# Kernel optimization log

Measured on AMD Instinct MI355X. Metric: run time of the kernel, lower is better.

The kernel has to match this reference:

```python
import jax, jax.numpy as jnp
import numpy as np

N_E = 8192
E_DIM = 256
BETA = 0.1


def setup_inputs() -> dict:
    key = jax.random.key(0)
    k1, k2 = jax.random.split(key)
    z = jax.random.normal(k1, (16, E_DIM, 2048), dtype=jnp.float32)  # B,C,L
    # embedding init: uniform(-1/n_e, 1/n_e)
    codebook = jax.random.uniform(k2, (N_E, E_DIM), dtype=jnp.float32,
                                  minval=-1.0 / N_E, maxval=1.0 / N_E)
    return {"z": z, "codebook": codebook}


def reference(z, codebook):
    B, C, L = z.shape
    zt = jnp.transpose(z, (0, 2, 1))          # B,L,C
    zf = zt.reshape(-1, C)                    # BL,C
    # squared-distance via expansion: |z|^2 + |e|^2 - 2 z.e
    d = (jnp.sum(zf * zf, axis=1, keepdims=True)
         + jnp.sum(codebook * codebook, axis=1)
         - 2.0 * jnp.einsum('bd,nd->bn', zf, codebook))  # BL,N
    inds = jnp.argmin(d, axis=1)              # BL
    z_q = codebook[inds].reshape(B, L, C)     # B,L,C
    sg = jax.lax.stop_gradient
    loss = (BETA * jnp.mean((sg(z_q) - zt) ** 2)
            + jnp.mean((z_q - sg(zt)) ** 2))
    # straight-through estimator
    z_q = zt + sg(z_q - zt)
    z_q = jnp.transpose(z_q, (0, 2, 1))       # B,C,L
    return z_q, loss, inds
```

## Files before the change

### kernel.cpp

```cpp
#include <hip/hip_runtime.h>
#include <math.h>

#define NE    8192
#define EDIM  256
#define LDIM  2048
#define BL    32768
#define ZQ_SIZE 8388608
#define LOSS_IDX ZQ_SIZE
#define INDS_OFF (ZQ_SIZE + 1)

#define BT_HI_F 0
#define BT_LO_F 1048576
#define PART_F  2097152
#define SZ_F    6291456
#define AT_LO_SH 8388608

typedef __attribute__((ext_vector_type(8))) short short8;
typedef __attribute__((ext_vector_type(16))) float float16v;

__device__ __forceinline__ unsigned short f2bf(float f) {
    unsigned u = __float_as_uint(f);
    return (unsigned short)((u + 0x7FFFu + ((u >> 16) & 1u)) >> 16);
}
__device__ __forceinline__ float bf2f(unsigned short h) {
    return __uint_as_float(((unsigned)h) << 16);
}
__device__ __forceinline__ void pmerge(ulonglong2& a, const ulonglong2 b) {
    unsigned long long lo = a.x < b.x ? a.x : b.x;
    unsigned long long hi = a.x < b.x ? b.x : a.x;
    unsigned long long s2 = a.y < b.y ? a.y : b.y;
    a.x = lo; a.y = s2 < hi ? s2 : hi;
}
__device__ __forceinline__ void gload_lds16(const void* g, void* l) {
    __builtin_amdgcn_global_load_lds(
        (const __attribute__((address_space(1))) unsigned int*)g,
        (__attribute__((address_space(3))) unsigned int*)l, 16, 0, 0);
}

__global__ void vq_bsplit_kernel(const float* __restrict__ cb, float* __restrict__ out) {
    unsigned short* Bth = (unsigned short*)(out + BT_HI_F);
    unsigned short* Btl = (unsigned short*)(out + BT_LO_F);
    const int oct = blockIdx.y;
    const int row = blockIdx.x * 256 + threadIdx.x;
    const float* src = cb + (size_t)row * EDIM + oct * 8;
    float v[8];
    *(float4*)&v[0] = *(const float4*)src;
    *(float4*)&v[4] = *(const float4*)(src + 4);
    short8 h8, l8;
    #pragma unroll
    for (int j = 0; j < 8; ++j) {
        unsigned short h = f2bf(v[j]);
        h8[j] = (short)h;
        l8[j] = (short)f2bf(v[j] - bf2f(h));
    }
    size_t o = ((size_t)(oct * NE + row)) << 3;
    *(short8*)(Bth + o) = h8;
    *(short8*)(Btl + o) = l8;
}

__global__ void vq_szsplit_kernel(const float* __restrict__ z, float* __restrict__ out,
                                  unsigned short* __restrict__ ws) {
    __shared__ double Sd[4][128];
    unsigned short* Ath = ws;
    unsigned short* Atl = ws + AT_LO_SH;
    const int t  = threadIdx.x;
    const int ql = t & 127;
    const int cq = t >> 7;
    const int q  = blockIdx.x * 128 + ql;
    if (q == 0 && cq == 0) out[LOSS_IDX] = 0.0f;
    const int b = q >> 11, l = q & 2047;
    const float* zb = z + (size_t)b * EDIM * LDIM + l;
    double acc = 0.0;
    #pragma unroll 2
    for (int og = cq * 8; og < cq * 8 + 8; ++og) {
        float v[8];
        #pragma unroll
        for (int j = 0; j < 8; ++j) v[j] = zb[(size_t)(og * 8 + j) * LDIM];
        short8 h8, l8;
        #pragma unroll
        for (int j = 0; j < 8; ++j) {
            unsigned u  = __float_as_uint(v[j]);
            unsigned hu = u & 0xFFFF0000u;
            float rem   = v[j] - __uint_as_float(hu);
            h8[j] = (short)(hu >> 16);
            l8[j] = (short)(__float_as_uint(rem) >> 16);
            double dv = (double)v[j];
            acc = fma(dv, dv, acc);
        }
        size_t o = ((size_t)og * BL + q) << 3;
        *(short8*)(Ath + o) = h8;
        *(short8*)(Atl + o) = l8;
    }
    Sd[cq][ql] = acc;
    __syncthreads();
    if (t < 128) {
        double s = Sd[0][t] + Sd[1][t] + Sd[2][t] + Sd[3][t];
        out[SZ_F + blockIdx.x * 128 + t] = (float)s;
    }
}

__global__ void vq_sz_kernel(const float* __restrict__ z, float* __restrict__ out) {
    const int q = blockIdx.x * 256 + threadIdx.x;
    if (q == 0) out[LOSS_IDX] = 0.0f;
    const int b = q >> 11, l = q & 2047;
    const float* zb = z + (size_t)b * EDIM * LDIM + l;
    double acc = 0.0;
    #pragma unroll 8
    for (int c = 0; c < EDIM; ++c) {
        double v = (double)zb[(size_t)c * LDIM];
        acc = fma(v, v, acc);
    }
    out[SZ_F + q] = (float)acc;
}

__global__ __launch_bounds__(512, 4) void vq_mfma_ws_kernel(
        const unsigned short* __restrict__ ws, float* __restrict__ out) {
    __shared__ __align__(16) unsigned short AhS[4 * 128 * 8];
    __shared__ __align__(16) unsigned short AlS[4 * 128 * 8];
    __shared__ __align__(16) unsigned short BhS[4 * 256 * 8];
    __shared__ __align__(16) unsigned short BlS[4 * 256 * 8];

    const unsigned short* Ath = ws;
    const unsigned short* Atl = ws + AT_LO_SH;
    const unsigned short* Bth = (const unsigned short*)(out + BT_HI_F);
    const unsigned short* Btl = (const unsigned short*)(out + BT_LO_F);
    const float* Szp = out + SZ_F;
    ulonglong2* part = (ulonglong2*)(out + PART_F);

    const int t    = threadIdx.x;
    const int lane = t & 63;
    const int wave = t >> 6;
    const int l31  = lane & 31;
    const int khal = lane >> 5;
    const int wm   = wave >> 2;
    const int wn   = wave & 3;

    const int q0 = (blockIdx.x >> 1) * 128;
    const int nh = blockIdx.x & 1;

    float szv2[2];
    #pragma unroll
    for (int ct = 0; ct < 2; ++ct)
        szv2[ct] = Szp[q0 + wm * 64 + ct * 32 + l31];

    float16v acc[2][2];
    unsigned long long k1r[2], k2r[2];
    #pragma unroll
    for (int ct = 0; ct < 2; ++ct) { k1r[ct] = ~0ull; k2r[ct] = ~0ull; }

    for (int cl = 0; cl < 16; ++cl) {
        const int n0c = nh * 4096 + cl * 256;
        #pragma unroll
        for (int rt = 0; rt < 2; ++rt)
            #pragma unroll
            for (int ct = 0; ct < 2; ++ct)
                #pragma unroll
                for (int e = 0; e < 16; ++e)
                    acc[rt][ct][e] = 0.f;

        for (int ks = 0; ks < 8; ++ks) {
            __syncthreads();
            #pragma unroll
            for (int i = 0; i < 2; ++i) {
                const int s   = wave * 2 + i;
                const int arr = s >> 3;
                const int oc  = (s >> 1) & 3;
                const int mh  = s & 1;
                const unsigned short* src = (arr ? Atl : Ath)
                    + ((size_t)((ks * 4 + oc) * BL + q0 + mh * 64 + lane) << 3);
                unsigned short* dst = (arr ? AlS : AhS)
                    + (((oc << 7) + mh * 64 + lane) << 3);
                gload_lds16(src, dst);
            }
            #pragma unroll
            for (int p = 0; p < 4; ++p) {
                const int s   = wave * 4 + p;
                const int arr = s >> 4;
                const int oc  = (s >> 2) & 3;
                const int seg = s & 3;
                const int og  = ks * 4 + oc;
                const unsigned short* src = (arr ? Btl : Bth)
                    + ((size_t)(og * NE + n0c + seg * 64 + lane) << 3);
                unsigned short* dst = (arr ? BlS : BhS)
                    + (((oc << 8) + seg * 64 + lane) << 3);
                gload_lds16(src, dst);
            }
            __syncthreads();
            #pragma unroll
            for (int c = 0; c < 2; ++c) {
                const int oct = c * 2 + khal;
                short8 cbh[2], cbl[2], qh[2], ql[2];
                #pragma unroll
                for (int rt = 0; rt < 2; ++rt) {
                    const int n = wn * 64 + rt * 32 + l31;
                    cbh[rt] = *(const short8*)&BhS[((oct << 8) + n) << 3];
                    cbl[rt] = *(const short8*)&BlS[((oct << 8) + n) << 3];
                }
                #pragma unroll
                for (int ct = 0; ct < 2; ++ct) {
                    const int m = wm * 64 + ct * 32 + l31;
                    qh[ct] = *(const short8*)&AhS[((oct << 7) + m) << 3];
                    ql[ct] = *(const short8*)&AlS[((oct << 7) + m) << 3];
                }
                #pragma unroll
                for (int rt = 0; rt < 2; ++rt)
                    #pragma unroll
                    for (int ct = 0; ct < 2; ++ct) {
                        acc[rt][ct] = __builtin_amdgcn_mfma_f32_32x32x16_bf16(cbh[rt], qh[ct], acc[rt][ct], 0, 0, 0);
                        acc[rt][ct] = __builtin_amdgcn_mfma_f32_32x32x16_bf16(cbl[rt], qh[ct], acc[rt][ct], 0, 0, 0);
                        acc[rt][ct] = __builtin_amdgcn_mfma_f32_32x32x16_bf16(cbh[rt], ql[ct], acc[rt][ct], 0, 0, 0);
                    }
            }
        }
        #pragma unroll
        for (int ct = 0; ct < 2; ++ct) {
            #pragma unroll
            for (int rt = 0; rt < 2; ++rt) {
                #pragma unroll
                for (int e = 0; e < 16; ++e) {
                    float s = fmaf(-2.0f, acc[rt][ct][e], szv2[ct]);
                    unsigned u = __float_as_uint(s);
                    unsigned mono = u ^ ((unsigned)(((int)u) >> 31) | 0x80000000u);
                    const int n = n0c + wn * 64 + rt * 32
                                + (e & 3) + 8 * (e >> 2) + 4 * khal;
                    unsigned long long k = ((unsigned long long)mono << 32) | (unsigned)n;
                    if (k < k1r[ct]) { k2r[ct] = k1r[ct]; k1r[ct] = k; }
                    else if (k < k2r[ct]) { k2r[ct] = k; }
                }
            }
        }
    }

    __syncthreads();
    ulonglong2* Sm = (ulonglong2*)AhS;
    #pragma unroll
    for (int ct = 0; ct < 2; ++ct) {
        unsigned long long k1 = k1r[ct], k2 = k2r[ct];
        unsigned long long o1 = __shfl_xor(k1, 32, 64);
        unsigned long long o2 = __shfl_xor(k2, 32, 64);
        unsigned long long lo = k1 < o1 ? k1 : o1;
        unsigned long long hi = k1 < o1 ? o1 : k1;
        k2 = k2 < o2 ? k2 : o2;
        k2 = k2 < hi ? k2 : hi;
        k1 = lo;
        if (khal == 0) {
            const int ql_ = wm * 64 + ct * 32 + l31;
            ulonglong2 v; v.x = k1; v.y = k2;
            Sm[(ql_ << 2) + wn] = v;
        }
    }
    __syncthreads();
    if (t < 128) {
        ulonglong2 p = Sm[(t << 2) + 0];
        pmerge(p, Sm[(t << 2) + 1]);
        pmerge(p, Sm[(t << 2) + 2]);
        pmerge(p, Sm[(t << 2) + 3]);
        part[(size_t)nh * BL + q0 + t] = p;
    }
}

__global__ __launch_bounds__(512, 4) void vq_mfma_kernel(
        const float* __restrict__ z, float* __restrict__ out) {
    __shared__ __align__(16) unsigned short AhS[4 * 128 * 8];
    __shared__ __align__(16) unsigned short AlS[4 * 128 * 8];
    __shared__ __align__(16) unsigned short BhS[4 * 256 * 8];
    __shared__ __align__(16) unsigned short BlS[4 * 256 * 8];

    const unsigned short* Bth = (const unsigned short*)(out + BT_HI_F);
    const unsigned short* Btl = (const unsigned short*)(out + BT_LO_F);
    const float* Szp = out + SZ_F;
    ulonglong2* part = (ulonglong2*)(out + PART_F);

    const int t    = threadIdx.x;
    const int lane = t & 63;
    const int wave = t >> 6;
    const int l31  = lane & 31;
    const int khal = lane >> 5;
    const int wm   = wave >> 2;
    const int wn   = wave & 3;

    const int q0 = (blockIdx.x >> 1) * 128;
    const int nh = blockIdx.x & 1;
    const int b  = q0 >> 11;
    const int l0 = q0 & 2047;
    const float* zbase = z + (size_t)b * (EDIM * LDIM) + l0;

    float szv2[2];
    #pragma unroll
    for (int ct = 0; ct < 2; ++ct)
        szv2[ct] = Szp[q0 + wm * 64 + ct * 32 + l31];

    const int am  = t & 127;
    const int aog = t >> 7;

    float16v acc[2][2];
    unsigned long long k1r[2], k2r[2];
    #pragma unroll
    for (int ct = 0; ct < 2; ++ct) { k1r[ct] = ~0ull; k2r[ct] = ~0ull; }

    for (int cl = 0; cl < 16; ++cl) {
        const int n0c = nh * 4096 + cl * 256;
        #pragma unroll
        for (int rt = 0; rt < 2; ++rt)
            #pragma unroll
            for (int ct = 0; ct < 2; ++ct)
                #pragma unroll
                for (int e = 0; e < 16; ++e)
                    acc[rt][ct][e] = 0.f;

        for (int ks = 0; ks < 8; ++ks) {
            const int kc = ks * 32;
            __syncthreads();
            {
                const float* asrc = zbase + (size_t)(kc + aog * 8) * LDIM + am;
                float av[8];
                #pragma unroll
                for (int j = 0; j < 8; ++j) av[j] = asrc[(size_t)j * LDIM];
                short8 h8, l8;
                #pragma unroll
                for (int j = 0; j < 8; ++j) {
                    unsigned u  = __float_as_uint(av[j]);
                    unsigned hu = u & 0xFFFF0000u;
                    float rem   = av[j] - __uint_as_float(hu);
                    h8[j] = (short)(hu >> 16);
                    l8[j] = (short)(__float_as_uint(rem) >> 16);
                }
                *(short8*)&AhS[((aog << 7) + am) << 3] = h8;
                *(short8*)&AlS[((aog << 7) + am) << 3] = l8;
            }
            #pragma unroll
            for (int p = 0; p < 4; ++p) {
                const int s   = wave * 4 + p;
                const int arr = s >> 4;
                const int oc  = (s >> 2) & 3;
                const int seg = s & 3;
                const int og  = ks * 4 + oc;
                const unsigned short* src = (arr ? Btl : Bth)
                    + ((size_t)(og * NE + n0c + seg * 64 + lane) << 3);
                unsigned short* dst = (arr ? BlS : BhS)
                    + (((oc << 8) + seg * 64 + lane) << 3);
                gload_lds16(src, dst);
            }
            __syncthreads();
            #pragma unroll
            for (int c = 0; c < 2; ++c) {
                const int oct = c * 2 + khal;
                short8 cbh[2], cbl[2], qh[2], ql[2];
                #pragma unroll
                for (int rt = 0; rt < 2; ++rt) {
                    const int n = wn * 64 + rt * 32 + l31;
                    cbh[rt] = *(const short8*)&BhS[((oct << 8) + n) << 3];
                    cbl[rt] = *(const short8*)&BlS[((oct << 8) + n) << 3];
                }
                #pragma unroll
                for (int ct = 0; ct < 2; ++ct) {
                    const int m = wm * 64 + ct * 32 + l31;
                    qh[ct] = *(const short8*)&AhS[((oct << 7) + m) << 3];
                    ql[ct] = *(const short8*)&AlS[((oct << 7) + m) << 3];
                }
                #pragma unroll
                for (int rt = 0; rt < 2; ++rt)
                    #pragma unroll
                    for (int ct = 0; ct < 2; ++ct) {
                        acc[rt][ct] = __builtin_amdgcn_mfma_f32_32x32x16_bf16(cbh[rt], qh[ct], acc[rt][ct], 0, 0, 0);
                        acc[rt][ct] = __builtin_amdgcn_mfma_f32_32x32x16_bf16(cbl[rt], qh[ct], acc[rt][ct], 0, 0, 0);
                        acc[rt][ct] = __builtin_amdgcn_mfma_f32_32x32x16_bf16(cbh[rt], ql[ct], acc[rt][ct], 0, 0, 0);
                    }
            }
        }
        #pragma unroll
        for (int ct = 0; ct < 2; ++ct) {
            #pragma unroll
            for (int rt = 0; rt < 2; ++rt) {
                #pragma unroll
                for (int e = 0; e < 16; ++e) {
                    float s = fmaf(-2.0f, acc[rt][ct][e], szv2[ct]);
                    unsigned u = __float_as_uint(s);
                    unsigned mono = u ^ ((unsigned)(((int)u) >> 31) | 0x80000000u);
                    const int n = n0c + wn * 64 + rt * 32
                                + (e & 3) + 8 * (e >> 2) + 4 * khal;
                    unsigned long long k = ((unsigned long long)mono << 32) | (unsigned)n;
                    if (k < k1r[ct]) { k2r[ct] = k1r[ct]; k1r[ct] = k; }
                    else if (k < k2r[ct]) { k2r[ct] = k; }
                }
            }
        }
    }

    __syncthreads();
    ulonglong2* Sm = (ulonglong2*)AhS;
    #pragma unroll
    for (int ct = 0; ct < 2; ++ct) {
        unsigned long long k1 = k1r[ct], k2 = k2r[ct];
        unsigned long long o1 = __shfl_xor(k1, 32, 64);
        unsigned long long o2 = __shfl_xor(k2, 32, 64);
        unsigned long long lo = k1 < o1 ? k1 : o1;
        unsigned long long hi = k1 < o1 ? o1 : k1;
        k2 = k2 < o2 ? k2 : o2;
        k2 = k2 < hi ? k2 : hi;
        k1 = lo;
        if (khal == 0) {
            const int ql_ = wm * 64 + ct * 32 + l31;
            ulonglong2 v; v.x = k1; v.y = k2;
            Sm[(ql_ << 2) + wn] = v;
        }
    }
    __syncthreads();
    if (t < 128) {
        ulonglong2 p = Sm[(t << 2) + 0];
        pmerge(p, Sm[(t << 2) + 1]);
        pmerge(p, Sm[(t << 2) + 2]);
        pmerge(p, Sm[(t << 2) + 3]);
        part[(size_t)nh * BL + q0 + t] = p;
    }
}

__global__ void vq_verify_kernel(const float* __restrict__ z,
                                 const float* __restrict__ cb,
                                 float* __restrict__ out) {
    const int t    = threadIdx.x;
    const int w    = t >> 6;
    const int lane = t & 63;
    const int q    = blockIdx.x * 4 + w;
    const int b    = q >> 11, l = q & 2047;
    const ulonglong2* part = (const ulonglong2*)(out + PART_F);
    ulonglong2 g = part[q];
    pmerge(g, part[(size_t)BL + q]);
    const int c1 = (int)(unsigned)(g.x & 0xFFFFFFFFull);
    const int c2 = (int)(unsigned)(g.y & 0xFFFFFFFFull);
    const float szq = out[SZ_F + q];
    const float* zb = z + (size_t)b * EDIM * LDIM + l;
    const float* r1 = cb + (size_t)c1 * EDIM;
    const float* r2 = cb + (size_t)c2 * EDIM;
    double d1 = 0.0, d2 = 0.0;
    #pragma unroll
    for (int j = 0; j < 4; ++j) {
        int d = lane + 64 * j;
        double zv = (double)zb[(size_t)d * LDIM];
        d1 = fma(zv, (double)r1[d], d1);
        d2 = fma(zv, (double)r2[d], d2);
    }
    #pragma unroll
    for (int off = 32; off; off >>= 1) {
        d1 += __shfl_xor(d1, off, 64);
        d2 += __shfl_xor(d2, off, 64);
    }
    if (lane == 0) {
        float s1 = fmaf(-2.0f, (float)d1, szq);
        float s2 = fmaf(-2.0f, (float)d2, szq);
        int win = (s1 < s2) ? c1 : (s2 < s1 ? c2 : (c1 < c2 ? c1 : c2));
        out[INDS_OFF + q] = (float)win;
    }
}

__global__ void vq_output_kernel(const float* __restrict__ z,
                                 const float* __restrict__ cb,
                                 float* __restrict__ out) {
    __shared__ float rows[32 * 257];
    __shared__ float wsum[4];
    const float* indsf = out + INDS_OFF;
    const int t  = threadIdx.x;
    const int i0 = blockIdx.x * 32;
    const int b  = i0 >> 11;
    const int l0 = i0 & 2047;
    {
        int r  = t >> 3;
        int fb = t & 7;
        int idx = (int)indsf[i0 + r];
        const float* crow = cb + (size_t)idx * EDIM;
        #pragma unroll
        for (int j = 0; j < 8; ++j) {
            int f = fb + 8 * j;
            float4 v = *(const float4*)(crow + 4 * f);
            float* dst = &rows[r * 257 + 4 * f];
            dst[0] = v.x; dst[1] = v.y; dst[2] = v.z; dst[3] = v.w;
        }
    }
    __syncthreads();
    const int l  = t & 31;
    const int c0 = t >> 5;
    const size_t base = (size_t)b * EDIM * LDIM + l0 + l;
    float lsum = 0.0f;
    #pragma unroll 4
    for (int cc = 0; cc < 32; ++cc) {
        int c = c0 + 8 * cc;
        float q  = rows[l * 257 + c];
        float zv = z[base + (size_t)c * LDIM];
        float d  = q - zv;
        out[base + (size_t)c * LDIM] = zv + d;
        lsum += d * d;
    }
    #pragma unroll
    for (int off = 32; off; off >>= 1) lsum += __shfl_xor(lsum, off, 64);
    if ((t & 63) == 0) wsum[t >> 6] = lsum;
    __syncthreads();
    if (t == 0) {
        float s = wsum[0] + wsum[1] + wsum[2] + wsum[3];
        atomicAdd(out + LOSS_IDX, s * (1.1f / (float)ZQ_SIZE));
    }
}

extern "C" void kernel_launch(void* const* d_in, const int* in_sizes, int n_in,
                              void* d_out, int out_size, void* d_ws, size_t ws_size,
                              hipStream_t stream) {
    const float* z  = (const float*)d_in[0];
    const float* cb = (const float*)d_in[1];
    float* out = (float*)d_out;

    const bool use_ws = (d_ws != nullptr) && (ws_size >= (size_t)33554432);

    vq_bsplit_kernel<<<dim3(32, 32),   dim3(256), 0, stream>>>(cb, out);
    if (use_ws) {
        unsigned short* ws = (unsigned short*)d_ws;
        vq_szsplit_kernel<<<dim3(256),     dim3(512), 0, stream>>>(z, out, ws);
        vq_mfma_ws_kernel<<<dim3(BL / 64), dim3(512), 0, stream>>>(ws, out);
    } else {
        vq_sz_kernel    <<<dim3(BL / 256), dim3(256), 0, stream>>>(z, out);
        vq_mfma_kernel  <<<dim3(BL / 64),  dim3(512), 0, stream>>>(z, out);
    }
    vq_verify_kernel<<<dim3(BL / 4),   dim3(256), 0, stream>>>(z, cb, out);
    vq_output_kernel<<<dim3(BL / 32),  dim3(256), 0, stream>>>(z, cb, out);
}
```

Baseline: 572.2 us.

## Triple-buffer LDS tiles with a single barrier per k-step in VQ MFMA kernel

Replaces the double-synchronized load/compute loop with a three-stage LDS ring buffer. Each k-substep now covers two octets, and the next stage's global-to-LDS copy is issued before computing on the current one. The code waits with a partial vmcnt plus one barrier, raises wave priority around the MFMA block, and fully unrolls the codebook chunk loop through macros. The goal is to hide global load latency and halve barrier count. In exchange it uses more LDS, which may reduce occupancy, and adds subtle indexing and wait-count logic across stages.

```diff
diff --git a/kernel.cpp b/kernel.cpp
--- a/kernel.cpp
+++ b/kernel.cpp
@@ -115,10 +115,7 @@
 
 __global__ __launch_bounds__(512, 4) void vq_mfma_ws_kernel(
         const unsigned short* __restrict__ ws, float* __restrict__ out) {
-    __shared__ __align__(16) unsigned short AhS[4 * 128 * 8];
-    __shared__ __align__(16) unsigned short AlS[4 * 128 * 8];
-    __shared__ __align__(16) unsigned short BhS[4 * 256 * 8];
-    __shared__ __align__(16) unsigned short BlS[4 * 256 * 8];
+    __shared__ __align__(16) unsigned short L[3 * 12288];
 
     const unsigned short* Ath = ws;
     const unsigned short* Atl = ws + AT_LO_SH;
@@ -137,102 +134,128 @@
 
     const int q0 = (blockIdx.x >> 1) * 128;
     const int nh = blockIdx.x & 1;
+    const int nh4096 = nh * 4096;
 
     float szv2[2];
     #pragma unroll
     for (int ct = 0; ct < 2; ++ct)
         szv2[ct] = Szp[q0 + wm * 64 + ct * 32 + l31];
 
+    const int a_arr = t >> 8;
+    const int a_oc2 = (t >> 7) & 1;
+    const int a_m   = t & 127;
+    const unsigned short* a_srcb = (a_arr ? Atl : Ath)
+        + ((size_t)(a_oc2 * BL + q0 + a_m) << 3);
+    unsigned short* a_dstb = L + a_arr * 2048 + (((a_oc2 << 7) + a_m) << 3);
+    const unsigned short* b_srcb[2];
+    unsigned short* b_dstb[2];
+    #pragma unroll
+    for (int p = 0; p < 2; ++p) {
+        const int idx = t + p * 512;
+        const int arr = idx >> 9;
+        const int oc2 = (idx >> 8) & 1;
+        const int n   = idx & 255;
+        b_srcb[p] = (arr ? Btl : Bth) + ((size_t)(oc2 * NE + n) << 3);
+        b_dstb[p] = L + 4096 + arr * 4096 + (((oc2 << 8) + n) << 3);
+    }
+
     float16v acc[2][2];
     unsigned long long k1r[2], k2r[2];
     #pragma unroll
     for (int ct = 0; ct < 2; ++ct) { k1r[ct] = ~0ull; k2r[ct] = ~0ull; }
 
-    for (int cl = 0; cl < 16; ++cl) {
-        const int n0c = nh * 4096 + cl * 256;
-        #pragma unroll
-        for (int rt = 0; rt < 2; ++rt)
-            #pragma unroll
-            for (int ct = 0; ct < 2; ++ct)
-                #pragma unroll
-                for (int e = 0; e < 16; ++e)
-                    acc[rt][ct][e] = 0.f;
-
-        for (int ks = 0; ks < 8; ++ks) {
-            __syncthreads();
-            #pragma unroll
-            for (int i = 0; i < 2; ++i) {
-                const int s   = wave * 2 + i;
-                const int arr = s >> 3;
-                const int oc  = (s >> 1) & 3;
-                const int mh  = s & 1;
-                const unsigned short* src = (arr ? Atl : Ath)
-                    + ((size_t)((ks * 4 + oc) * BL + q0 + mh * 64 + lane) << 3);
-                unsigned short* dst = (arr ? AlS : AhS)
-                    + (((oc << 7) + mh * 64 + lane) << 3);
-                gload_lds16(src, dst);
-            }
-            #pragma unroll
-            for (int p = 0; p < 4; ++p) {
-                const int s   = wave * 4 + p;
-                const int arr = s >> 4;
-                const int oc  = (s >> 2) & 3;
-                const int seg = s & 3;
-                const int og  = ks * 4 + oc;
-                const unsigned short* src = (arr ? Btl : Bth)
-                    + ((size_t)(og * NE + n0c + seg * 64 + lane) << 3);
-                unsigned short* dst = (arr ? BlS : BhS)
-                    + (((oc << 8) + seg * 64 + lane) << 3);
-                gload_lds16(src, dst);
-            }
-            __syncthreads();
-            #pragma unroll
-            for (int c = 0; c < 2; ++c) {
-                const int oct = c * 2 + khal;
-                short8 cbh[2], cbl[2], qh[2], ql[2];
-                #pragma unroll
-                for (int rt = 0; rt < 2; ++rt) {
-                    const int n = wn * 64 + rt * 32 + l31;
-                    cbh[rt] = *(const short8*)&BhS[((oct << 8) + n) << 3];
-                    cbl[rt] = *(const short8*)&BlS[((oct << 8) + n) << 3];
-                }
-                #pragma unroll
-                for (int ct = 0; ct < 2; ++ct) {
-                    const int m = wm * 64 + ct * 32 + l31;
-                    qh[ct] = *(const short8*)&AhS[((oct << 7) + m) << 3];
-                    ql[ct] = *(const short8*)&AlS[((oct << 7) + m) << 3];
-                }
-                #pragma unroll
-                for (int rt = 0; rt < 2; ++rt)
-                    #pragma unroll
-                    for (int ct = 0; ct < 2; ++ct) {
-                        acc[rt][ct] = __builtin_amdgcn_mfma_f32_32x32x16_bf16(cbh[rt], qh[ct], acc[rt][ct], 0, 0, 0);
-                        acc[rt][ct] = __builtin_amdgcn_mfma_f32_32x32x16_bf16(cbl[rt], qh[ct], acc[rt][ct], 0, 0, 0);
-                        acc[rt][ct] = __builtin_amdgcn_mfma_f32_32x32x16_bf16(cbh[rt], ql[ct], acc[rt][ct], 0, 0, 0);
-                    }
-            }
-        }
-        #pragma unroll
-        for (int ct = 0; ct < 2; ++ct) {
-            #pragma unroll
-            for (int rt = 0; rt < 2; ++rt) {
-                #pragma unroll
-                for (int e = 0; e < 16; ++e) {
-                    float s = fmaf(-2.0f, acc[rt][ct][e], szv2[ct]);
-                    unsigned u = __float_as_uint(s);
-                    unsigned mono = u ^ ((unsigned)(((int)u) >> 31) | 0x80000000u);
-                    const int n = n0c + wn * 64 + rt * 32
-                                + (e & 3) + 8 * (e >> 2) + 4 * khal;
-                    unsigned long long k = ((unsigned long long)mono << 32) | (unsigned)n;
-                    if (k < k1r[ct]) { k2r[ct] = k1r[ct]; k1r[ct] = k; }
-                    else if (k < k2r[ct]) { k2r[ct] = k; }
-                }
-            }
-        }
-    }
-
-    __syncthreads();
-    ulonglong2* Sm = (ulonglong2*)AhS;
+#define VQ_STAGE(OG0, N0CS, BUFN) do { \
+    gload_lds16(a_srcb + (((size_t)(OG0) * BL) << 3), a_dstb + (BUFN) * 12288); \
+    gload_lds16(b_srcb[0] + ((((size_t)(OG0) * NE) + (N0CS)) << 3), b_dstb[0] + (BUFN) * 12288); \
+    gload_lds16(b_srcb[1] + ((((size_t)(OG0) * NE) + (N0CS)) << 3), b_dstb[1] + (BUFN) * 12288); \
+} while (0)
+
+#define VQ_CMP(BUFC) do { \
+    const unsigned short* base_ = L + (BUFC) * 12288; \
+    short8 cbh_[2], cbl_[2], qh_[2], ql_[2]; \
+    _Pragma("unroll") \
+    for (int rt_ = 0; rt_ < 2; ++rt_) { \
+        const int n_ = wn * 64 + rt_ * 32 + l31; \
+        cbh_[rt_] = *(const short8*)(base_ + 4096 + (((khal << 8) + n_) << 3)); \
+        cbl_[rt_] = *(const short8*)(base_ + 8192 + (((khal << 8) + n_) << 3)); \
+    } \
+    _Pragma("unroll") \
+    for (int ct_ = 0; ct_ < 2; ++ct_) { \
+        const int m_ = wm * 64 + ct_ * 32 + l31; \
+        qh_[ct_] = *(const short8*)(base_ + (((khal << 7) + m_) << 3)); \
+        ql_[ct_] = *(const short8*)(base_ + 2048 + (((khal << 7) + m_) << 3)); \
+    } \
+    __builtin_amdgcn_s_setprio(1); \
+    _Pragma("unroll") \
+    for (int rt_ = 0; rt_ < 2; ++rt_) \
+        _Pragma("unroll") \
+        for (int ct_ = 0; ct_ < 2; ++ct_) { \
+            acc[rt_][ct_] = __builtin_amdgcn_mfma_f32_32x32x16_bf16(cbh_[rt_], qh_[ct_], acc[rt_][ct_], 0, 0, 0); \
+            acc[rt_][ct_] = __builtin_amdgcn_mfma_f32_32x32x16_bf16(cbl_[rt_], qh_[ct_], acc[rt_][ct_], 0, 0, 0); \
+            acc[rt_][ct_] = __builtin_amdgcn_mfma_f32_32x32x16_bf16(cbh_[rt_], ql_[ct_], acc[rt_][ct_], 0, 0, 0); \
+        } \
+    __builtin_amdgcn_s_setprio(0); \
+} while (0)
+
+#define VQ_SUB(TT, JJ, N0CS) do { \
+    VQ_STAGE(((2 * ((TT) + 1)) & 31), (N0CS), (((JJ) * 16 + (TT) + 1) % 3)); \
+    asm volatile("s_waitcnt vmcnt(3)" ::: "memory"); \
+    __builtin_amdgcn_s_barrier(); \
+    __builtin_amdgcn_sched_barrier(0); \
+    VQ_CMP((((JJ) * 16 + (TT)) % 3)); \
+} while (0)
+
+#define VQ_CLBODY(JJ) do { \
+    const int n0c_  = nh4096 + cl * 256; \
+    const int n0cn_ = nh4096 + ((cl + 1) & 15) * 256; \
+    _Pragma("unroll") \
+    for (int rt_ = 0; rt_ < 2; ++rt_) \
+        _Pragma("unroll") \
+        for (int ct_ = 0; ct_ < 2; ++ct_) \
+            _Pragma("unroll") \
+            for (int e_ = 0; e_ < 16; ++e_) \
+                acc[rt_][ct_][e_] = 0.f; \
+    VQ_SUB( 0, JJ, n0c_);  VQ_SUB( 1, JJ, n0c_);  VQ_SUB( 2, JJ, n0c_);  VQ_SUB( 3, JJ, n0c_); \
+    VQ_SUB( 4, JJ, n0c_);  VQ_SUB( 5, JJ, n0c_);  VQ_SUB( 6, JJ, n0c_);  VQ_SUB( 7, JJ, n0c_); \
+    VQ_SUB( 8, JJ, n0c_);  VQ_SUB( 9, JJ, n0c_);  VQ_SUB(10, JJ, n0c_);  VQ_SUB(11, JJ, n0c_); \
+    VQ_SUB(12, JJ, n0c_);  VQ_SUB(13, JJ, n0c_);  VQ_SUB(14, JJ, n0c_);  VQ_SUB(15, JJ, n0cn_); \
+    _Pragma("unroll") \
+    for (int ct_ = 0; ct_ < 2; ++ct_) { \
+        _Pragma("unroll") \
+        for (int rt_ = 0; rt_ < 2; ++rt_) { \
+            _Pragma("unroll") \
+            for (int e_ = 0; e_ < 16; ++e_) { \
+                float s_ = fmaf(-2.0f, acc[rt_][ct_][e_], szv2[ct_]);  \
+                unsigned u_ = __float_as_uint(s_); \
+                unsigned mono_ = u_ ^ ((unsigned)(((int)u_) >> 31) | 0x80000000u); \
+                const int n_ = n0c_ + wn * 64 + rt_ * 32 \
+                             + (e_ & 3) + 8 * (e_ >> 2) + 4 * khal; \
+                unsigned long long k_ = ((unsigned long long)mono_ << 32) | (unsigned)n_; \
+                if (k_ < k1r[ct_]) { k2r[ct_] = k1r[ct_]; k1r[ct_] = k_; } \
+                else if (k_ < k2r[ct_]) { k2r[ct_] = k_; } \
+            } \
+        } \
+    } \
+} while (0)
+
+    VQ_STAGE(0, nh4096, 0);
+
+    int cl = 0;
+    #pragma unroll 1
+    for (int clb = 0; clb < 15; clb += 3) {
+        VQ_CLBODY(0); ++cl;
+        VQ_CLBODY(1); ++cl;
+        VQ_CLBODY(2); ++cl;
+    }
+    VQ_CLBODY(0);
+
+#undef VQ_STAGE
+#undef VQ_CMP
+#undef VQ_SUB
+#undef VQ_CLBODY
+
+    __syncthreads();
+    ulonglong2* Sm = (ulonglong2*)L;
     #pragma unroll
     for (int ct = 0; ct < 2; ++ct) {
         unsigned long long k1 = k1r[ct], k2 = k2r[ct];
```

Result: slower. 628.3 us (+9.8%).
